# Optimization experiments

Hardware: AMD Instinct MI355X
Metric: run time of the kernel (lower is better)

## Reference

```python
import jax, jax.numpy as jnp
import numpy as np

B, N, D = 8, 2048, 512  # batch, input_dim (tokens), weight_dim


def setup_inputs() -> dict:
    key = jax.random.key(0)
    ks = jax.random.split(key, 7)
    return {
        "query": jax.random.normal(ks[0], (B, N, D), dtype=jnp.float32),
        "key": jax.random.normal(ks[1], (B, N, D), dtype=jnp.float32),
        "value": jax.random.normal(ks[2], (B, N, D), dtype=jnp.float32),
        "W_query": jax.random.normal(ks[3], (D, D), dtype=jnp.float32),
        "W_key": jax.random.normal(ks[4], (D, D), dtype=jnp.float32),
        "W_value": jax.random.normal(ks[5], (D, D), dtype=jnp.float32),
        "self_importance": jnp.zeros((N,), dtype=jnp.float32),
    }


def reference(query, key, value, W_query, W_key, W_value, self_importance):
    d = W_query.shape[0]
    q = jnp.einsum("bnd,de->bne", query, W_query)
    k = jnp.einsum("bnd,de->bne", key, W_key)
    v = jnp.einsum("bnd,de->bne", value, W_value)
    scores = jnp.einsum("bqe,bke->bqk", q, k) / jnp.sqrt(jnp.float32(d))
    # diagonal self-importance bias: eye(N) * clamp(exp(s), max=3)
    importance = jnp.minimum(jnp.exp(self_importance), 3.0)  # [N]
    n = scores.shape[1]
    idx = jnp.arange(n)
    scores = scores.at[:, idx, idx].add(importance)
    attn = jax.nn.softmax(scores, axis=-1)  # [B, N, N]
    entropy_loss = -jnp.mean(jnp.sum(attn * jnp.log(attn + 1e-10), axis=-1))
    out = jnp.einsum("bqk,bke->bqe", attn, v)
    return (out, attn, entropy_loss)
```

## Files before the change

kernel.cpp:

```cpp
#include <hip/hip_runtime.h>
#include <math.h>

#define BB 8
#define NN 2048
#define DD 512

typedef _Float16 halfT;
typedef _Float16 half8 __attribute__((ext_vector_type(8)));
typedef _Float16 half4 __attribute__((ext_vector_type(4)));
typedef float f32x4 __attribute__((ext_vector_type(4)));
typedef float f32x16 __attribute__((ext_vector_type(16)));

#define GLOAD16(gp, sp) __builtin_amdgcn_global_load_lds( \
    (const __attribute__((address_space(1))) void*)(gp), \
    (__attribute__((address_space(3))) void*)(sp), 16, 0, 0)

__global__ __launch_bounds__(256) void wsplit_kernel(
    const float* __restrict__ Wq, const float* __restrict__ Wk, const float* __restrict__ Wv,
    _Float16* __restrict__ qhT, _Float16* __restrict__ qlT,
    _Float16* __restrict__ khT, _Float16* __restrict__ klT,
    _Float16* __restrict__ vhT)
{
    __shared__ float t[64][65];
    const int z = blockIdx.z;
    const float* W = (z == 0) ? Wq : ((z == 1) ? Wk : Wv);
    _Float16* Ph = (z == 0) ? qhT : ((z == 1) ? khT : vhT);
    _Float16* Pl = (z == 0) ? qlT : ((z == 1) ? klT : nullptr);
    const int bx = blockIdx.x * 64, by = blockIdx.y * 64;
    const int tid = threadIdx.x;
    #pragma unroll
    for (int i = 0; i < 16; ++i) {
        const int idx = i * 256 + tid;
        const int r = idx >> 6, c = idx & 63;
        t[r][c] = W[(long)(by + r) * 512 + bx + c];
    }
    __syncthreads();
    #pragma unroll
    for (int i = 0; i < 16; ++i) {
        const int idx = i * 256 + tid;
        const int r = idx >> 6, c = idx & 63;
        const float v = t[c][r];
        const _Float16 h = (_Float16)v;
        const long o = (long)(bx + r) * 512 + by + c;
        Ph[o] = h;
        if (z < 2) Pl[o] = (_Float16)(v - (float)h);
    }
}

__global__ __launch_bounds__(256) void projqk_kernel(
    const float* __restrict__ Af0, const float* __restrict__ Af1,
    const _Float16* __restrict__ B0h, const _Float16* __restrict__ B0l,
    const _Float16* __restrict__ B1h, const _Float16* __restrict__ B1l,
    _Float16* __restrict__ O0h, _Float16* __restrict__ O0l,
    _Float16* __restrict__ O1h, _Float16* __restrict__ O1l)
{
    __shared__ __align__(16) _Float16 smem[4 * 128 * 32];
    _Float16* Ah = smem;
    _Float16* Bh = smem + 4096;
    _Float16* Al = smem + 8192;
    _Float16* Bl = smem + 12288;

    const int z = blockIdx.z;
    const float* Af = z ? Af1 : Af0;
    const _Float16* Bgh = z ? B1h : B0h;
    const _Float16* Bgl = z ? B1l : B0l;
    _Float16* Oh = z ? O1h : O0h;
    _Float16* Ol = z ? O1l : O0l;

    const int tid  = threadIdx.x;
    const int lane = tid & 63;
    const int w    = tid >> 6;
    const int wr   = w >> 1, wc = w & 1;
    const int bm   = blockIdx.y * 128, bn = blockIdx.x * 128;

    f32x4 acc[4][4];
    #pragma unroll
    for (int i = 0; i < 4; ++i)
        #pragma unroll
        for (int j = 0; j < 4; ++j) acc[i][j] = (f32x4)0.0f;

    for (int k0 = 0; k0 < DD; k0 += 32) {
        #pragma unroll
        for (int i = 0; i < 2; ++i) {
            const int c   = i * 256 + w * 64 + lane;
            const int row = c >> 2, sl = c & 3;
            const long g  = (long)(bn + row) * DD + k0 + sl * 8;
            const int lb  = (i * 256 + w * 64) * 8;
            GLOAD16(Bgh + g, Bh + lb);
            GLOAD16(Bgl + g, Bl + lb);
        }
        #pragma unroll
        for (int i = 0; i < 4; ++i) {
            const int c = tid + i * 256;
            const int row = c >> 3, q4 = c & 7;
            const float4 v = *(const float4*)(Af + (long)(bm + row) * DD + k0 + q4 * 4);
            half4 h;
            h[0] = (_Float16)v.x; h[1] = (_Float16)v.y;
            h[2] = (_Float16)v.z; h[3] = (_Float16)v.w;
            *(half4*)&Ah[row * 32 + q4 * 4] = h;
            half4 l;
            l[0] = (_Float16)(v.x - (float)h[0]);
            l[1] = (_Float16)(v.y - (float)h[1]);
            l[2] = (_Float16)(v.z - (float)h[2]);
            l[3] = (_Float16)(v.w - (float)h[3]);
            *(half4*)&Al[row * 32 + q4 * 4] = l;
        }
        __syncthreads();

        half8 ah[4], bh[4], al[4], bl[4];
        #pragma unroll
        for (int f = 0; f < 4; ++f) {
            const int ar = wr * 64 + f * 16 + (lane & 15);
            const int ao = ar * 32 + ((lane >> 4) << 3);
            ah[f] = *(const half8*)&Ah[ao];
            al[f] = *(const half8*)&Al[ao];
            const int br = wc * 64 + f * 16 + (lane & 15);
            const int bo = br * 32 + ((lane >> 4) << 3);
            bh[f] = *(const half8*)&Bh[bo];
            bl[f] = *(const half8*)&Bl[bo];
        }
        #pragma unroll
        for (int i = 0; i < 4; ++i)
            #pragma unroll
            for (int j = 0; j < 4; ++j) {
                acc[i][j] = __builtin_amdgcn_mfma_f32_16x16x32_f16(ah[i], bh[j], acc[i][j], 0, 0, 0);
                acc[i][j] = __builtin_amdgcn_mfma_f32_16x16x32_f16(ah[i], bl[j], acc[i][j], 0, 0, 0);
                acc[i][j] = __builtin_amdgcn_mfma_f32_16x16x32_f16(al[i], bh[j], acc[i][j], 0, 0, 0);
            }
        __syncthreads();
    }

    #pragma unroll
    for (int i = 0; i < 4; ++i) {
        const int rb = bm + wr * 64 + i * 16 + ((lane >> 4) << 2);
        #pragma unroll
        for (int j = 0; j < 4; ++j) {
            const int gc = bn + wc * 64 + j * 16 + (lane & 15);
            #pragma unroll
            for (int r = 0; r < 4; ++r) {
                const float vv = acc[i][j][r];
                const _Float16 h = (_Float16)vv;
                const long o = (long)(rb + r) * DD + gc;
                Oh[o] = h;
                Ol[o] = (_Float16)(vv - (float)h);
            }
        }
    }
}

__global__ __launch_bounds__(256) void vproj_kernel(
    const float* __restrict__ Af, const _Float16* __restrict__ Bgh,
    _Float16* __restrict__ Oh)
{
    __shared__ __align__(16) _Float16 smem[2 * 128 * 32];
    _Float16* Ah = smem;
    _Float16* Bh = smem + 4096;

    const int tid  = threadIdx.x;
    const int lane = tid & 63;
    const int w    = tid >> 6;
    const int wr   = w >> 1, wc = w & 1;
    const int bm   = blockIdx.y * 128, bn = blockIdx.x * 128;

    f32x4 acc[4][4];
    #pragma unroll
    for (int i = 0; i < 4; ++i)
        #pragma unroll
        for (int j = 0; j < 4; ++j) acc[i][j] = (f32x4)0.0f;

    for (int k0 = 0; k0 < DD; k0 += 32) {
        #pragma unroll
        for (int i = 0; i < 2; ++i) {
            const int c   = i * 256 + w * 64 + lane;
            const int row = c >> 2, sl = c & 3;
            const long g  = (long)(bn + row) * DD + k0 + sl * 8;
            const int lb  = (i * 256 + w * 64) * 8;
            GLOAD16(Bgh + g, Bh + lb);
        }
        #pragma unroll
        for (int i = 0; i < 4; ++i) {
            const int c = tid + i * 256;
            const int row = c >> 3, q4 = c & 7;
            const float4 v = *(const float4*)(Af + (long)(bm + row) * DD + k0 + q4 * 4);
            half4 h;
            h[0] = (_Float16)v.x; h[1] = (_Float16)v.y;
            h[2] = (_Float16)v.z; h[3] = (_Float16)v.w;
            *(half4*)&Ah[row * 32 + q4 * 4] = h;
        }
        __syncthreads();

        half8 ah[4], bh[4];
        #pragma unroll
        for (int f = 0; f < 4; ++f) {
            const int ar = wr * 64 + f * 16 + (lane & 15);
            ah[f] = *(const half8*)&Ah[ar * 32 + ((lane >> 4) << 3)];
            const int br = wc * 64 + f * 16 + (lane & 15);
            bh[f] = *(const half8*)&Bh[br * 32 + ((lane >> 4) << 3)];
        }
        #pragma unroll
        for (int i = 0; i < 4; ++i)
            #pragma unroll
            for (int j = 0; j < 4; ++j)
                acc[i][j] = __builtin_amdgcn_mfma_f32_16x16x32_f16(ah[i], bh[j], acc[i][j], 0, 0, 0);
        __syncthreads();
    }

    #pragma unroll
    for (int i = 0; i < 4; ++i) {
        const int rb = bm + wr * 64 + i * 16 + ((lane >> 4) << 2);
        #pragma unroll
        for (int j = 0; j < 4; ++j) {
            const int gc = bn + wc * 64 + j * 16 + (lane & 15);
            half4 hv;
            #pragma unroll
            for (int r = 0; r < 4; ++r) hv[r] = (_Float16)acc[i][j][r];
            const int b = rb >> 11, rIn = rb & 2047;
            *(half4*)&Oh[((long)b * 512 + gc) * 2048 + rIn] = hv;
        }
    }
}

__global__ __launch_bounds__(512, 2) void scores256_kernel(
    const halfT* __restrict__ qh, const halfT* __restrict__ ql,
    const halfT* __restrict__ kh, const halfT* __restrict__ kl,
    float* __restrict__ C, const float* __restrict__ si, float scale)
{
    extern __shared__ __align__(16) char smem[];

    const int tid  = threadIdx.x;
    const int lane = tid & 63;
    const int w    = tid >> 6;
    const int wr   = w >> 2, wc = w & 3;

    int flat = (blockIdx.z << 6) | (blockIdx.y << 3) | blockIdx.x;
    flat = ((flat & 7) << 6) | (flat >> 3);
    const int bx = flat & 7, by = (flat >> 3) & 7, bz = flat >> 6;
    const int bm = by * 256, bn = bx * 256;

    const long zoff = (long)bz * NN * DD;
    const halfT* A_h = qh + zoff;
    const halfT* A_l = ql + zoff;
    const halfT* B_h = kh + zoff;
    const halfT* B_l = kl + zoff;

    const int s_row   = w * 16 + (lane >> 2);
    const int s_chunk = (lane & 3) ^ ((lane >> 3) & 3);
    const long gA = (long)(bm + s_row) * DD + s_chunk * 8;
    const long gB = (long)(bn + s_row) * DD + s_chunk * 8;
    const int ldst = w * 1024;
    const long rstep = (long)128 * DD;

    auto stage = [&](char* buf, int t) {
        const long kk = (long)t * 32;
        GLOAD16(A_h + gA + kk,         buf + ldst);
        GLOAD16(A_h + gA + rstep + kk, buf + 8192 + ldst);
        GLOAD16(A_l + gA + kk,         buf + 16384 + ldst);
        GLOAD16(A_l + gA + rstep + kk, buf + 16384 + 8192 + ldst);
        GLOAD16(B_h + gB + kk,         buf + 32768 + ldst);
        GLOAD16(B_h + gB + rstep + kk, buf + 32768 + 8192 + ldst);
        GLOAD16(B_l + gB + kk,         buf + 49152 + ldst);
        GLOAD16(B_l + gB + rstep + kk, buf + 49152 + 8192 + ldst);
    };

    const int frow = lane & 31;
    const int fgr  = lane >> 5;

    f32x16 acc[4][2];
    #pragma unroll
    for (int m = 0; m < 4; ++m)
        #pragma unroll
        for (int n = 0; n < 2; ++n) acc[m][n] = (f32x16)0.0f;

    stage(smem, 0);
    asm volatile("s_waitcnt vmcnt(0)" ::: "memory");
    __builtin_amdgcn_s_barrier();
    __builtin_amdgcn_sched_barrier(0);

    for (int t = 0; t < 16; ++t) {
        char* cur = smem + (size_t)(t & 1) * 65536;
        char* nxt = smem + (size_t)((t + 1) & 1) * 65536;

        if (t < 15) stage(nxt, t + 1);

        auto fr = [&](const char* unit, int row, int kh) -> half8 {
            const int g = kh * 2 + fgr;
            const int phys = g ^ ((row >> 1) & 3);
            return *(const half8*)(unit + row * 64 + phys * 16);
        };

        half8 a_[4][2], bh_[2][2];
        #pragma unroll
        for (int kh2 = 0; kh2 < 2; ++kh2) {
            #pragma unroll
            for (int n = 0; n < 2; ++n)
                bh_[n][kh2] = fr(cur + 32768, wc * 64 + n * 32 + frow, kh2);
            #pragma unroll
            for (int m = 0; m < 4; ++m)
                a_[m][kh2] = fr(cur, wr * 128 + m * 32 + frow, kh2);
        }
        __builtin_amdgcn_s_setprio(1);
        #pragma unroll
        for (int m = 0; m < 4; ++m)
            #pragma unroll
            for (int n = 0; n < 2; ++n)
                #pragma unroll
                for (int kh2 = 0; kh2 < 2; ++kh2)
                    acc[m][n] = __builtin_amdgcn_mfma_f32_32x32x16_f16(a_[m][kh2], bh_[n][kh2], acc[m][n], 0, 0, 0);
        __builtin_amdgcn_s_setprio(0);

        half8 bl_[2][2];
        #pragma unroll
        for (int kh2 = 0; kh2 < 2; ++kh2)
            #pragma unroll
            for (int n = 0; n < 2; ++n)
                bl_[n][kh2] = fr(cur + 49152, wc * 64 + n * 32 + frow, kh2);
        __builtin_amdgcn_s_setprio(1);
        #pragma unroll
        for (int m = 0; m < 4; ++m)
            #pragma unroll
            for (int n = 0; n < 2; ++n)
                #pragma unroll
                for (int kh2 = 0; kh2 < 2; ++kh2)
                    acc[m][n] = __builtin_amdgcn_mfma_f32_32x32x16_f16(a_[m][kh2], bl_[n][kh2], acc[m][n], 0, 0, 0);
        __builtin_amdgcn_s_setprio(0);

        __builtin_amdgcn_s_setprio(1);
        #pragma unroll
        for (int m = 0; m < 4; ++m) {
            half8 al0 = fr(cur + 16384, wr * 128 + m * 32 + frow, 0);
            half8 al1 = fr(cur + 16384, wr * 128 + m * 32 + frow, 1);
            #pragma unroll
            for (int n = 0; n < 2; ++n) {
                acc[m][n] = __builtin_amdgcn_mfma_f32_32x32x16_f16(al0, bh_[n][0], acc[m][n], 0, 0, 0);
                acc[m][n] = __builtin_amdgcn_mfma_f32_32x32x16_f16(al1, bh_[n][1], acc[m][n], 0, 0, 0);
            }
        }
        __builtin_amdgcn_s_setprio(0);

        if (t < 15) {
            asm volatile("s_waitcnt vmcnt(0)" ::: "memory");
            __builtin_amdgcn_s_barrier();
        }
    }

    float* Cz = C + (long)bz * NN * NN;
    const int rbias = 4 * (lane >> 5);
    #pragma unroll
    for (int m = 0; m < 4; ++m) {
        #pragma unroll
        for (int n = 0; n < 2; ++n) {
            const int gc = bn + wc * 64 + n * 32 + (lane & 31);
            #pragma unroll
            for (int reg = 0; reg < 16; ++reg) {
                const int gr = bm + wr * 128 + m * 32 + (reg & 3) + 8 * (reg >> 2) + rbias;
                float vv = acc[m][n][reg] * scale;
                if (gr == gc) vv += fminf(expf(si[gr]), 3.0f);
                Cz[(long)gr * NN + gc] = vv;
            }
        }
    }
}

__global__ __launch_bounds__(512, 2) void av_kernel(
    const halfT* __restrict__ P, const halfT* __restrict__ V,
    float* __restrict__ O)
{
    extern __shared__ __align__(16) char smem[];

    const int tid  = threadIdx.x;
    const int lane = tid & 63;
    const int w    = tid >> 6;
    const int wr   = w >> 2, wc = w & 3;

    int flat = (blockIdx.z << 5) | (blockIdx.y << 2) | blockIdx.x;
    flat = ((flat & 7) << 5) | (flat >> 3);
    const int nx = flat & 3, my = (flat >> 2) & 7, bz = flat >> 5;
    const int bm = my * 256, bn = nx * 128;

    const halfT* A = P + (long)bz * NN * NN;
    const halfT* B = V + (long)bz * DD * NN;

    const int s_row   = w * 16 + (lane >> 2);
    const int s_chunk = (lane & 3) ^ ((lane >> 3) & 3);
    const long gA = (long)(bm + s_row) * NN + s_chunk * 8;
    const long gB = (long)(bn + s_row) * NN + s_chunk * 8;
    const int ldst = w * 1024;
    const long rstep = (long)128 * NN;

    auto stage = [&](char* buf, int t) {
        const long kk = (long)t * 32;
        GLOAD16(A + gA + kk,         buf + ldst);
        GLOAD16(A + gA + rstep + kk, buf + 8192 + ldst);
        GLOAD16(B + gB + kk,         buf + 16384 + ldst);
    };

    const int frow = lane & 31;
    const int fgr  = lane >> 5;

    f32x16 acc[4];
    #pragma unroll
    for (int m = 0; m < 4; ++m) acc[m] = (f32x16)0.0f;

    stage(smem, 0);
    asm volatile("s_waitcnt vmcnt(0)" ::: "memory");
    __builtin_amdgcn_s_barrier();
    __builtin_amdgcn_sched_barrier(0);

    for (int t = 0; t < 64; ++t) {
        char* cur = smem + (size_t)(t & 1) * 24576;
        char* nxt = smem + (size_t)((t + 1) & 1) * 24576;

        if (t < 63) stage(nxt, t + 1);

        auto fr = [&](const char* unit, int row, int kh) -> half8 {
            const int g = kh * 2 + fgr;
            const int phys = g ^ ((row >> 1) & 3);
            return *(const half8*)(unit + row * 64 + phys * 16);
        };

        half8 a_[4][2], b_[2];
        #pragma unroll
        for (int kh2 = 0; kh2 < 2; ++kh2) {
            b_[kh2] = fr(cur + 16384, wc * 32 + frow, kh2);
            #pragma unroll
            for (int m = 0; m < 4; ++m)
                a_[m][kh2] = fr(cur, wr * 128 + m * 32 + frow, kh2);
        }
        __builtin_amdgcn_s_setprio(1);
        #pragma unroll
        for (int m = 0; m < 4; ++m)
            #pragma unroll
            for (int kh2 = 0; kh2 < 2; ++kh2)
                acc[m] = __builtin_amdgcn_mfma_f32_32x32x16_f16(a_[m][kh2], b_[kh2], acc[m], 0, 0, 0);
        __builtin_amdgcn_s_setprio(0);

        if (t < 63) {
            asm volatile("s_waitcnt vmcnt(0)" ::: "memory");
            __builtin_amdgcn_s_barrier();
        }
    }

    float* Oz = O + (long)bz * NN * DD;
    const int rbias = 4 * (lane >> 5);
    const int gc = bn + wc * 32 + (lane & 31);
    #pragma unroll
    for (int m = 0; m < 4; ++m) {
        #pragma unroll
        for (int reg = 0; reg < 16; ++reg) {
            const int gr = bm + wr * 128 + m * 32 + (reg & 3) + 8 * (reg >> 2) + rbias;
            Oz[(long)gr * DD + gc] = acc[m][reg];
        }
    }
}

__global__ __launch_bounds__(256) void softmax_entropy_kernel(
    float* __restrict__ attn, _Float16* __restrict__ ah, float* __restrict__ partials)
{
    __shared__ float red[4];
    const long row = blockIdx.x;
    float* p = attn + row * (long)NN;
    _Float16* ph = ah + row * (long)NN;
    const int tid = threadIdx.x;
    const int base = tid * 8;

    float4 va = *(const float4*)(p + base);
    float4 vb = *(const float4*)(p + base + 4);
    float v[8] = {va.x, va.y, va.z, va.w, vb.x, vb.y, vb.z, vb.w};

    float m = v[0];
    #pragma unroll
    for (int i = 1; i < 8; ++i) m = fmaxf(m, v[i]);
    #pragma unroll
    for (int o = 32; o; o >>= 1) m = fmaxf(m, __shfl_xor(m, o, 64));
    if ((tid & 63) == 0) red[tid >> 6] = m;
    __syncthreads();
    m = fmaxf(fmaxf(red[0], red[1]), fmaxf(red[2], red[3]));

    float t[8];
    float s = 0.f;
    #pragma unroll
    for (int i = 0; i < 8; ++i) { t[i] = v[i] - m; v[i] = expf(t[i]); s += v[i]; }
    #pragma unroll
    for (int o = 32; o; o >>= 1) s += __shfl_xor(s, o, 64);
    __syncthreads();
    if ((tid & 63) == 0) red[tid >> 6] = s;
    __syncthreads();
    s = red[0] + red[1] + red[2] + red[3];

    const float inv = 1.0f / s;
    const float lns = logf(s);
    float e = 0.f;
    float pv[8];
    #pragma unroll
    for (int i = 0; i < 8; ++i) {
        pv[i] = v[i] * inv;
        e = fmaf(pv[i], t[i] - lns, e);
    }
    *(float4*)(p + base)     = make_float4(pv[0], pv[1], pv[2], pv[3]);
    *(float4*)(p + base + 4) = make_float4(pv[4], pv[5], pv[6], pv[7]);
    half8 h;
    #pragma unroll
    for (int i = 0; i < 8; ++i) h[i] = (_Float16)pv[i];
    *(half8*)(ph + base) = h;

    #pragma unroll
    for (int o = 32; o; o >>= 1) e += __shfl_xor(e, o, 64);
    __syncthreads();
    if ((tid & 63) == 0) red[tid >> 6] = e;
    __syncthreads();
    if (tid == 0) partials[row] = red[0] + red[1] + red[2] + red[3];
}

__global__ __launch_bounds__(256) void ent_reduce_kernel(
    const float* __restrict__ partials, float* __restrict__ ent)
{
    __shared__ float red[4];
    float s = 0.f;
    for (int i = threadIdx.x; i < BB * NN; i += 256) s += partials[i];
    #pragma unroll
    for (int o = 32; o; o >>= 1) s += __shfl_xor(s, o, 64);
    if ((threadIdx.x & 63) == 0) red[threadIdx.x >> 6] = s;
    __syncthreads();
    if (threadIdx.x == 0)
        *ent = -(red[0] + red[1] + red[2] + red[3]) / (float)(BB * NN);
}

extern "C" void kernel_launch(void* const* d_in, const int* in_sizes, int n_in,
                              void* d_out, int out_size, void* d_ws, size_t ws_size,
                              hipStream_t stream) {
    const float* query = (const float*)d_in[0];
    const float* key   = (const float*)d_in[1];
    const float* value = (const float*)d_in[2];
    const float* Wq    = (const float*)d_in[3];
    const float* Wk    = (const float*)d_in[4];
    const float* Wv    = (const float*)d_in[5];
    const float* si    = (const float*)d_in[6];

    float* out  = (float*)d_out;
    float* attn = out + (size_t)BB * NN * DD;
    float* ent  = attn + (size_t)BB * NN * NN;

    const size_t NK = (size_t)BB * NN * DD;
    _Float16* ws16 = (_Float16*)d_ws;
    _Float16* qh = ws16;
    _Float16* ql = qh + NK;
    _Float16* kh = ql + NK;
    _Float16* kl = kh + NK;
    _Float16* vT = kl + NK;
    _Float16* WqhT = vT + NK;
    _Float16* WqlT = WqhT + DD * DD;
    _Float16* WkhT = WqlT + DD * DD;
    _Float16* WklT = WkhT + DD * DD;
    _Float16* WvhT = WklT + DD * DD;
    float* partials = (float*)(WvhT + DD * DD);
    _Float16* attn_h = ws16;

    const dim3 blk(256);
    const float inv_sqrt_d = 0.044194173824159216f;

    wsplit_kernel<<<dim3(8, 8, 3), blk, 0, stream>>>(Wq, Wk, Wv,
        WqhT, WqlT, WkhT, WklT, WvhT);

    projqk_kernel<<<dim3(4, 128, 2), blk, 0, stream>>>(
        query, key, WqhT, WqlT, WkhT, WklT, qh, ql, kh, kl);
    vproj_kernel<<<dim3(4, 128, 1), blk, 0, stream>>>(value, WvhT, vT);

    scores256_kernel<<<dim3(8, 8, 8), dim3(512), 131072, stream>>>(
        qh, ql, kh, kl, attn, si, inv_sqrt_d);

    softmax_entropy_kernel<<<dim3(BB * NN), blk, 0, stream>>>(attn, attn_h, partials);
    ent_reduce_kernel<<<dim3(1), blk, 0, stream>>>(partials, ent);

    av_kernel<<<dim3(4, 8, 8), dim3(512), 49152, stream>>>(attn_h, vT, out);
}
```

Before: 335.0 us.

## Rework Q/K projection pipeline and switch scores/AV MFMAs to 16x16 tiles

```diff
diff --git a/kernel.cpp b/kernel.cpp
--- a/kernel.cpp
+++ b/kernel.cpp
@@ -9,7 +9,6 @@
 typedef _Float16 half8 __attribute__((ext_vector_type(8)));
 typedef _Float16 half4 __attribute__((ext_vector_type(4)));
 typedef float f32x4 __attribute__((ext_vector_type(4)));
-typedef float f32x16 __attribute__((ext_vector_type(16)));
 
 #define GLOAD16(gp, sp) __builtin_amdgcn_global_load_lds( \
     (const __attribute__((address_space(1))) void*)(gp), \
@@ -47,25 +46,169 @@
     }
 }
 
-__global__ __launch_bounds__(256) void projqk_kernel(
-    const float* __restrict__ Af0, const float* __restrict__ Af1,
-    const _Float16* __restrict__ B0h, const _Float16* __restrict__ B0l,
-    const _Float16* __restrict__ B1h, const _Float16* __restrict__ B1l,
-    _Float16* __restrict__ O0h, _Float16* __restrict__ O0l,
-    _Float16* __restrict__ O1h, _Float16* __restrict__ O1l)
+__global__ __launch_bounds__(512, 2) void projqk_kernel(
+    const float* __restrict__ X0, const float* __restrict__ X1,
+    const halfT* __restrict__ B0h, const halfT* __restrict__ B0l,
+    const halfT* __restrict__ B1h, const halfT* __restrict__ B1l,
+    halfT* __restrict__ O0h, halfT* __restrict__ O0l,
+    halfT* __restrict__ O1h, halfT* __restrict__ O1l)
 {
-    __shared__ __align__(16) _Float16 smem[4 * 128 * 32];
+    extern __shared__ __align__(16) char smem[];
+
+    const int tid  = threadIdx.x;
+    const int lane = tid & 63;
+    const int w    = tid >> 6;
+    const int wr   = w >> 1, wc = w & 1;
+
+    const int h = blockIdx.x;
+    const int L = ((h & 7) << 6) | (h >> 3);
+    const int z  = L >> 8;
+    const int nx = L & 3, my = (L >> 2) & 63;
+    const int bm = my * 256, bn = nx * 128;
+
+    const float* X = z ? X1 : X0;
+    const halfT* Bgh = z ? B1h : B0h;
+    const halfT* Bgl = z ? B1l : B0l;
+    halfT* Oh = z ? O1h : O0h;
+    halfT* Ol = z ? O1l : O0l;
+
+    const int b_row   = w * 16 + (lane >> 2);
+    const int b_chunk = (lane & 3) ^ ((lane >> 3) & 3);
+    const long gB = (long)(bn + b_row) * DD + b_chunk * 8;
+    const int ldstB = w * 1024;
+
+    const int a_row0 = tid >> 2;
+    const int a_gc   = tid & 3;
+    const int a_phys = a_gc ^ ((a_row0 >> 1) & 3);
+    const long gA0 = (long)(bm + a_row0) * DD + a_gc * 8;
+    const long gA1 = (long)(bm + a_row0 + 128) * DD + a_gc * 8;
+    const int aOff0 = a_row0 * 64 + a_phys * 16;
+    const int aOff1 = (a_row0 + 128) * 64 + a_phys * 16;
+
+    float ar[16];
+    auto loadA = [&](int t) {
+        const long kk = (long)t * 32;
+        *(float4*)&ar[0]  = *(const float4*)(X + gA0 + kk);
+        *(float4*)&ar[4]  = *(const float4*)(X + gA0 + kk + 4);
+        *(float4*)&ar[8]  = *(const float4*)(X + gA1 + kk);
+        *(float4*)&ar[12] = *(const float4*)(X + gA1 + kk + 4);
+    };
+    auto stageB = [&](char* buf, int t) {
+        const long kk = (long)t * 32;
+        GLOAD16(Bgh + gB + kk, buf + 32768 + ldstB);
+        GLOAD16(Bgl + gB + kk, buf + 40960 + ldstB);
+    };
+    auto writeA = [&](char* buf) {
+        half8 h0, l0, h1, l1;
+        #pragma unroll
+        for (int i = 0; i < 8; ++i) {
+            const _Float16 hh = (_Float16)ar[i];
+            h0[i] = hh; l0[i] = (_Float16)(ar[i] - (float)hh);
+        }
+        #pragma unroll
+        for (int i = 0; i < 8; ++i) {
+            const _Float16 hh = (_Float16)ar[8 + i];
+            h1[i] = hh; l1[i] = (_Float16)(ar[8 + i] - (float)hh);
+        }
+        *(half8*)(buf + aOff0)         = h0;
+        *(half8*)(buf + 16384 + aOff0) = l0;
+        *(half8*)(buf + aOff1)         = h1;
+        *(half8*)(buf + 16384 + aOff1) = l1;
+    };
+
+    const int lr  = lane & 15;
+    const int q16 = lane >> 4;
+    const int frag = lr * 64 + ((q16 ^ ((lr >> 1) & 3)) << 4);
+    const int abase = wr * 4096 + frag;
+    const int bbase = wc * 4096 + frag;
+
+    f32x4 acc[4][4];
+    #pragma unroll
+    for (int i = 0; i < 4; ++i)
+        #pragma unroll
+        for (int j = 0; j < 4; ++j) acc[i][j] = (f32x4)0.0f;
+
+    loadA(0);
+    stageB(smem, 0);
+    writeA(smem);
+    asm volatile("s_waitcnt vmcnt(0) lgkmcnt(0)" ::: "memory");
+    __builtin_amdgcn_s_barrier();
+    __builtin_amdgcn_sched_barrier(0);
+
+    for (int t = 0; t < 16; ++t) {
+        char* cur = smem + (size_t)(t & 1) * 49152;
+        char* nxt = smem + (size_t)((t + 1) & 1) * 49152;
+        const bool pf = (t < 15);
+
+        if (pf) { loadA(t + 1); stageB(nxt, t + 1); }
+
+        half8 ah[4], bh[4], bl[4];
+        #pragma unroll
+        for (int m = 0; m < 4; ++m)
+            ah[m] = *(const half8*)(cur + abase + m * 1024);
+        #pragma unroll
+        for (int j = 0; j < 4; ++j)
+            bh[j] = *(const half8*)(cur + 32768 + bbase + j * 1024);
+        __builtin_amdgcn_s_setprio(1);
+        #pragma unroll
+        for (int m = 0; m < 4; ++m)
+            #pragma unroll
+            for (int j = 0; j < 4; ++j)
+                acc[m][j] = __builtin_amdgcn_mfma_f32_16x16x32_f16(ah[m], bh[j], acc[m][j], 0, 0, 0);
+        __builtin_amdgcn_s_setprio(0);
+
+        #pragma unroll
+        for (int j = 0; j < 4; ++j)
+            bl[j] = *(const half8*)(cur + 40960 + bbase + j * 1024);
+        __builtin_amdgcn_s_setprio(1);
+        #pragma unroll
+        for (int m = 0; m < 4; ++m)
+            #pragma unroll
+            for (int j = 0; j < 4; ++j)
+                acc[m][j] = __builtin_amdgcn_mfma_f32_16x16x32_f16(ah[m], bl[j], acc[m][j], 0, 0, 0);
+        __builtin_amdgcn_s_setprio(0);
+
+        __builtin_amdgcn_s_setprio(1);
+        #pragma unroll
+        for (int m = 0; m < 4; ++m) {
+            const half8 al = *(const half8*)(cur + 16384 + abase + m * 1024);
+            #pragma unroll
+            for (int j = 0; j < 4; ++j)
+                acc[m][j] = __builtin_amdgcn_mfma_f32_16x16x32_f16(al, bh[j], acc[m][j], 0, 0, 0);
+        }
+        __builtin_amdgcn_s_setprio(0);
+
+        if (pf) writeA(nxt);
+        asm volatile("s_waitcnt vmcnt(0) lgkmcnt(0)" ::: "memory");
+        __builtin_amdgcn_s_barrier();
+        __builtin_amdgcn_sched_barrier(0);
+    }
+
+    #pragma unroll
+    for (int m = 0; m < 4; ++m) {
+        const int rb = bm + wr * 64 + m * 16 + (q16 << 2);
+        #pragma unroll
+        for (int j = 0; j < 4; ++j) {
+            const int gc = bn + wc * 64 + j * 16 + lr;
+            #pragma unroll
+            for (int r = 0; r < 4; ++r) {
+                const float vv = acc[m][j][r];
+                const _Float16 hh = (_Float16)vv;
+                const long o = (long)(rb + r) * DD + gc;
+                Oh[o] = hh;
+                Ol[o] = (_Float16)(vv - (float)hh);
+            }
+        }
+    }
+}
+
+__global__ __launch_bounds__(256) void vproj_kernel(
+    const float* __restrict__ Af, const _Float16* __restrict__ Bgh,
+    _Float16* __restrict__ Oh)
+{
+    __shared__ __align__(16) _Float16 smem[2 * 128 * 32];
     _Float16* Ah = smem;
     _Float16* Bh = smem + 4096;
-    _Float16* Al = smem + 8192;
-    _Float16* Bl = smem + 12288;
-
-    const int z = blockIdx.z;
-    const float* Af = z ? Af1 : Af0;
-    const _Float16* Bgh = z ? B1h : B0h;
-    const _Float16* Bgl = z ? B1l : B0l;
-    _Float16* Oh = z ? O1h : O0h;
-    _Float16* Ol = z ? O1l : O0l;
 
     const int tid  = threadIdx.x;
     const int lane = tid & 63;
@@ -87,7 +230,6 @@
             const long g  = (long)(bn + row) * DD + k0 + sl * 8;
             const int lb  = (i * 256 + w * 64) * 8;
             GLOAD16(Bgh + g, Bh + lb);
-            GLOAD16(Bgl + g, Bl + lb);
         }
         #pragma unroll
         for (int i = 0; i < 4; ++i) {
@@ -98,104 +240,16 @@
             h[0] = (_Float16)v.x; h[1] = (_Float16)v.y;
             h[2] = (_Float16)v.z; h[3] = (_Float16)v.w;
             *(half4*)&Ah[row * 32 + q4 * 4] = h;
-            half4 l;
-            l[0] = (_Float16)(v.x - (float)h[0]);
-            l[1] = (_Float16)(v.y - (float)h[1]);
-            l[2] = (_Float16)(v.z - (float)h[2]);
-            l[3] = (_Float16)(v.w - (float)h[3]);
-            *(half4*)&Al[row * 32 + q4 * 4] = l;
         }
         __syncthreads();
 
-        half8 ah[4], bh[4], al[4], bl[4];
+        half8 ah[4], bh[4];
         #pragma unroll
         for (int f = 0; f < 4; ++f) {
-            const int ar = wr * 64 + f * 16 + (lane & 15);
-            const int ao = ar * 32 + ((lane >> 4) << 3);
-            ah[f] = *(const half8*)&Ah[ao];
-            al[f] = *(const half8*)&Al[ao];
-            const int br = wc * 64 + f * 16 + (lane & 15);
-            const int bo = br * 32 + ((lane >> 4) << 3);
-            bh[f] = *(const half8*)&Bh[bo];
-            bl[f] = *(const half8*)&Bl[bo];
-        }
-        #pragma unroll
-        for (int i = 0; i < 4; ++i)
-            #pragma unroll
-            for (int j = 0; j < 4; ++j) {
-                acc[i][j] = __builtin_amdgcn_mfma_f32_16x16x32_f16(ah[i], bh[j], acc[i][j], 0, 0, 0);
-                acc[i][j] = __builtin_amdgcn_mfma_f32_16x16x32_f16(ah[i], bl[j], acc[i][j], 0, 0, 0);
-                acc[i][j] = __builtin_amdgcn_mfma_f32_16x16x32_f16(al[i], bh[j], acc[i][j], 0, 0, 0);
-            }
-        __syncthreads();
-    }
-
-    #pragma unroll
-    for (int i = 0; i < 4; ++i) {
-        const int rb = bm + wr * 64 + i * 16 + ((lane >> 4) << 2);
-        #pragma unroll
-        for (int j = 0; j < 4; ++j) {
-            const int gc = bn + wc * 64 + j * 16 + (lane & 15);
-            #pragma unroll
-            for (int r = 0; r < 4; ++r) {
-                const float vv = acc[i][j][r];
-                const _Float16 h = (_Float16)vv;
-                const long o = (long)(rb + r) * DD + gc;
-                Oh[o] = h;
-                Ol[o] = (_Float16)(vv - (float)h);
-            }
-        }
-    }
-}
-
-__global__ __launch_bounds__(256) void vproj_kernel(
-    const float* __restrict__ Af, const _Float16* __restrict__ Bgh,
-    _Float16* __restrict__ Oh)
-{
-    __shared__ __align__(16) _Float16 smem[2 * 128 * 32];
-    _Float16* Ah = smem;
-    _Float16* Bh = smem + 4096;
-
-    const int tid  = threadIdx.x;
-    const int lane = tid & 63;
-    const int w    = tid >> 6;
-    const int wr   = w >> 1, wc = w & 1;
-    const int bm   = blockIdx.y * 128, bn = blockIdx.x * 128;
-
-    f32x4 acc[4][4];
-    #pragma unroll
-    for (int i = 0; i < 4; ++i)
-        #pragma unroll
-        for (int j = 0; j < 4; ++j) acc[i][j] = (f32x4)0.0f;
-
-    for (int k0 = 0; k0 < DD; k0 += 32) {
-        #pragma unroll
-        for (int i = 0; i < 2; ++i) {
-            const int c   = i * 256 + w * 64 + lane;
-            const int row = c >> 2, sl = c & 3;
-            const long g  = (long)(bn + row) * DD + k0 + sl * 8;
-            const int lb  = (i * 256 + w * 64) * 8;
-            GLOAD16(Bgh + g, Bh + lb);
-        }
-        #pragma unroll
-        for (int i = 0; i < 4; ++i) {
-            const int c = tid + i * 256;
-            const int row = c >> 3, q4 = c & 7;
-            const float4 v = *(const float4*)(Af + (long)(bm + row) * DD + k0 + q4 * 4);
-            half4 h;
-            h[0] = (_Float16)v.x; h[1] = (_Float16)v.y;
-            h[2] = (_Float16)v.z; h[3] = (_Float16)v.w;
-            *(half4*)&Ah[row * 32 + q4 * 4] = h;
-        }
-        __syncthreads();
-
-        half8 ah[4], bh[4];
-        #pragma unroll
-        for (int f = 0; f < 4; ++f) {
-            const int ar = wr * 64 + f * 16 + (lane & 15);
-            ah[f] = *(const half8*)&Ah[ar * 32 + ((lane >> 4) << 3)];
-            const int br = wc * 64 + f * 16 + (lane & 15);
-            bh[f] = *(const half8*)&Bh[br * 32 + ((lane >> 4) << 3)];
+            const int arr = wr * 64 + f * 16 + (lane & 15);
+            ah[f] = *(const half8*)&Ah[arr * 32 + ((lane >> 4) << 3)];
+            const int brr = wc * 64 + f * 16 + (lane & 15);
+            bh[f] = *(const half8*)&Bh[brr * 32 + ((lane >> 4) << 3)];
         }
         #pragma unroll
         for (int i = 0; i < 4; ++i)
@@ -262,19 +316,22 @@
         GLOAD16(B_l + gB + rstep + kk, buf + 49152 + 8192 + ldst);
     };
 
-    const int frow = lane & 31;
-    const int fgr  = lane >> 5;
-
-    f32x16 acc[4][2];
-    #pragma unroll
-    for (int m = 0; m < 4; ++m)
-        #pragma unroll
-        for (int n = 0; n < 2; ++n) acc[m][n] = (f32x16)0.0f;
+    const int lr   = lane & 15;
+    const int q16  = lane >> 4;
+    const int fswz = (lr >> 1) & 3;
+    const int frag = lr * 64 + ((q16 ^ fswz) << 4);
+    const int abase = wr * 8192 + frag;
+    const int bbase = wc * 4096 + frag;
+
+    f32x4 acc[8][4];
+    #pragma unroll
+    for (int m = 0; m < 8; ++m)
+        #pragma unroll
+        for (int n = 0; n < 4; ++n) acc[m][n] = (f32x4)0.0f;
 
     stage(smem, 0);
     asm volatile("s_waitcnt vmcnt(0)" ::: "memory");
     __builtin_amdgcn_s_barrier();
-    __builtin_amdgcn_sched_barrier(0);
 
     for (int t = 0; t < 16; ++t) {
         char* cur = smem + (size_t)(t & 1) * 65536;
@@ -282,58 +339,39 @@
 
         if (t < 15) stage(nxt, t + 1);
 
-        auto fr = [&](const char* unit, int row, int kh) -> half8 {
-            const int g = kh * 2 + fgr;
-            const int phys = g ^ ((row >> 1) & 3);
-            return *(const half8*)(unit + row * 64 + phys * 16);
-        };
-
-        half8 a_[4][2], bh_[2][2];
-        #pragma unroll
-        for (int kh2 = 0; kh2 < 2; ++kh2) {
-            #pragma unroll
-            for (int n = 0; n < 2; ++n)
-                bh_[n][kh2] = fr(cur + 32768, wc * 64 + n * 32 + frow, kh2);
-            #pragma unroll
-            for (int m = 0; m < 4; ++m)
-                a_[m][kh2] = fr(cur, wr * 128 + m * 32 + frow, kh2);
-        }
+        half8 ah[8], bh[4], bl[4];
+        #pragma unroll
+        for (int n = 0; n < 4; ++n)
+            bh[n] = *(const half8*)(cur + 32768 + bbase + n * 1024);
+        #pragma unroll
+        for (int m = 0; m < 8; ++m)
+            ah[m] = *(const half8*)(cur + abase + m * 1024);
         __builtin_amdgcn_s_setprio(1);
         #pragma unroll
-        for (int m = 0; m < 4; ++m)
-            #pragma unroll
-            for (int n = 0; n < 2; ++n)
-                #pragma unroll
-                for (int kh2 = 0; kh2 < 2; ++kh2)
-                    acc[m][n] = __builtin_amdgcn_mfma_f32_32x32x16_f16(a_[m][kh2], bh_[n][kh2], acc[m][n], 0, 0, 0);
+        for (int m = 0; m < 8; ++m)
+            #pragma unroll
+            for (int n = 0; n < 4; ++n)
+                acc[m][n] = __builtin_amdgcn_mfma_f32_16x16x32_f16(ah[m], bh[n], acc[m][n], 0, 0, 0);
         __builtin_amdgcn_s_setprio(0);
 
-        half8 bl_[2][2];
-        #pragma unroll
-        for (int kh2 = 0; kh2 < 2; ++kh2)
-            #pragma unroll
-            for (int n = 0; n < 2; ++n)
-                bl_[n][kh2] = fr(cur + 49152, wc * 64 + n * 32 + frow, kh2);
+        #pragma unroll
+        for (int n = 0; n < 4; ++n)
+            bl[n] = *(const half8*)(cur + 49152 + bbase + n * 1024);
         __builtin_amdgcn_s_setprio(1);
         #pragma unroll
-        for (int m = 0; m < 4; ++m)
-            #pragma unroll
-            for (int n = 0; n < 2; ++n)
-                #pragma unroll
-                for (int kh2 = 0; kh2 < 2; ++kh2)
-                    acc[m][n] = __builtin_amdgcn_mfma_f32_32x32x16_f16(a_[m][kh2], bl_[n][kh2], acc[m][n], 0, 0, 0);
+        for (int m = 0; m < 8; ++m)
+            #pragma unroll
+            for (int n = 0; n < 4; ++n)
+                acc[m][n] = __builtin_amdgcn_mfma_f32_16x16x32_f16(ah[m], bl[n], acc[m][n], 0, 0, 0);
         __builtin_amdgcn_s_setprio(0);
 
         __builtin_amdgcn_s_setprio(1);
         #pragma unroll
-        for (int m = 0; m < 4; ++m) {
-            half8 al0 = fr(cur + 16384, wr * 128 + m * 32 + frow, 0);
-            half8 al1 = fr(cur + 16384, wr * 128 + m * 32 + frow, 1);
-            #pragma unroll
-            for (int n = 0; n < 2; ++n) {
-                acc[m][n] = __builtin_amdgcn_mfma_f32_32x32x16_f16(al0, bh_[n][0], acc[m][n], 0, 0, 0);
-                acc[m][n] = __builtin_amdgcn_mfma_f32_32x32x16_f16(al1, bh_[n][1], acc[m][n], 0, 0, 0);
-            }
+        for (int m = 0; m < 8; ++m) {
+            const half8 al = *(const half8*)(cur + 16384 + abase + m * 1024);
+            #pragma unroll
+            for (int n = 0; n < 4; ++n)
+                acc[m][n] = __builtin_amdgcn_mfma_f32_16x16x32_f16(al, bh[n], acc[m][n], 0, 0, 0);
         }
         __builtin_amdgcn_s_setprio(0);
 
@@ -344,16 +382,16 @@
     }
 
     float* Cz = C + (long)bz * NN * NN;
-    const int rbias = 4 * (lane >> 5);
-    #pragma unroll
-    for (int m = 0; m < 4; ++m) {
-        #pragma unroll
-        for (int n = 0; n < 2; ++n) {
-            const int gc = bn + wc * 64 + n * 32 + (lane & 31);
-            #pragma unroll
-            for (int reg = 0; reg < 16; ++reg) {
-                const int gr = bm + wr * 128 + m * 32 + (reg & 3) + 8 * (reg >> 2) + rbias;
-                float vv = acc[m][n][reg] * scale;
+    #pragma unroll
+    for (int m = 0; m < 8; ++m) {
+        const int rb = bm + wr * 128 + m * 16 + ((lane >> 4) << 2);
+        #pragma unroll
+        for (int n = 0; n < 4; ++n) {
+            const int gc = bn + wc * 64 + n * 16 + (lane & 15);
+            #pragma unroll
+            for (int r = 0; r < 4; ++r) {
+                const int gr = rb + r;
+                float vv = acc[m][n][r] * scale;
                 if (gr == gc) vv += fminf(expf(si[gr]), 3.0f);
                 Cz[(long)gr * NN + gc] = vv;
             }
@@ -370,9 +408,9 @@
     const int tid  = threadIdx.x;
     const int lane = tid & 63;
     const int w    = tid >> 6;
-    const int wr   = w >> 2, wc = w & 3;
-
-    int flat = (blockIdx.z << 5) | (blockIdx.y << 2) | blockIdx.x;
+    const int wr   = w >> 1, wc = w & 1;
+
+    int flat = blockIdx.x;
     flat = ((flat & 7) << 5) | (flat >> 3);
     const int nx = flat & 3, my = (flat >> 2) & 7, bz = flat >> 5;
     const int bm = my * 256, bn = nx * 128;
@@ -394,12 +432,17 @@
         GLOAD16(B + gB + kk,         buf + 16384 + ldst);
     };
 
-    const int frow = lane & 31;
-    const int fgr  = lane >> 5;
-
-    f32x16 acc[4];
-    #pragma unroll
-    for (int m = 0; m < 4; ++m) acc[m] = (f32x16)0.0f;
+    const int lr  = lane & 15;
+    const int q16 = lane >> 4;
+    const int frag = lr * 64 + ((q16 ^ ((lr >> 1) & 3)) << 4);
+    const int abase = wr * 4096 + frag;
+    const int bbase = wc * 4096 + frag;
+
+    f32x4 acc[4][4];
+    #pragma unroll
+    for (int m = 0; m < 4; ++m)
+        #pragma unroll
+        for (int j = 0; j < 4; ++j) acc[m][j] = (f32x4)0.0f;
 
     stage(smem, 0);
     asm volatile("s_waitcnt vmcnt(0)" ::: "memory");
@@ -412,26 +455,19 @@
 
         if (t < 63) stage(nxt, t + 1);
 
-        auto fr = [&](const char* unit, int row, int kh) -> half8 {
-            const int g = kh * 2 + fgr;
-            const int phys = g ^ ((row >> 1) & 3);
-            return *(const half8*)(unit + row * 64 + phys * 16);
-        };
-
-        half8 a_[4][2], b_[2];
-        #pragma unroll
-        for (int kh2 = 0; kh2 < 2; ++kh2) {
-            b_[kh2] = fr(cur + 16384, wc * 32 + frow, kh2);
-            #pragma unroll
-            for (int m = 0; m < 4; ++m)
-                a_[m][kh2] = fr(cur, wr * 128 + m * 32 + frow, kh2);
-        }
+        half8 ah[4], bh[4];
+        #pragma unroll
+        for (int m = 0; m < 4; ++m)
+            ah[m] = *(const half8*)(cur + abase + m * 1024);
+        #pragma unroll
+        for (int j = 0; j < 4; ++j)
+            bh[j] = *(const half8*)(cur + 16384 + bbase + j * 1024);
         __builtin_amdgcn_s_setprio(1);
         #pragma unroll
         for (int m = 0; m < 4; ++m)
             #pragma unroll
-            for (int kh2 = 0; kh2 < 2; ++kh2)
-                acc[m] = __builtin_amdgcn_mfma_f32_32x32x16_f16(a_[m][kh2], b_[kh2], acc[m], 0, 0, 0);
+            for (int j = 0; j < 4; ++j)
+                acc[m][j] = __builtin_amdgcn_mfma_f32_16x16x32_f16(ah[m], bh[j], acc[m][j], 0, 0, 0);
         __builtin_amdgcn_s_setprio(0);
 
         if (t < 63) {
@@ -441,14 +477,15 @@
     }
 
     float* Oz = O + (long)bz * NN * DD;
-    const int rbias = 4 * (lane >> 5);
-    const int gc = bn + wc * 32 + (lane & 31);
     #pragma unroll
     for (int m = 0; m < 4; ++m) {
-        #pragma unroll
-        for (int reg = 0; reg < 16; ++reg) {
-            const int gr = bm + wr * 128 + m * 32 + (reg & 3) + 8 * (reg >> 2) + rbias;
-            Oz[(long)gr * DD + gc] = acc[m][reg];
+        const int rb = bm + wr * 64 + m * 16 + (q16 << 2);
+        #pragma unroll
+        for (int j = 0; j < 4; ++j) {
+            const int gc = bn + wc * 64 + j * 16 + lr;
+            #pragma unroll
+            for (int r = 0; r < 4; ++r)
+                Oz[(long)(rb + r) * DD + gc] = acc[m][j][r];
         }
     }
 }
@@ -561,7 +598,7 @@
     wsplit_kernel<<<dim3(8, 8, 3), blk, 0, stream>>>(Wq, Wk, Wv,
         WqhT, WqlT, WkhT, WklT, WvhT);
 
-    projqk_kernel<<<dim3(4, 128, 2), blk, 0, stream>>>(
+    projqk_kernel<<<dim3(512), dim3(512), 98304, stream>>>(
         query, key, WqhT, WqlT, WkhT, WklT, qh, ql, kh, kl);
     vproj_kernel<<<dim3(4, 128, 1), blk, 0, stream>>>(value, WvhT, vT);
 
@@ -571,5 +608,5 @@
     softmax_entropy_kernel<<<dim3(BB * NN), blk, 0, stream>>>(attn, attn_h, partials);
     ent_reduce_kernel<<<dim3(1), blk, 0, stream>>>(partials, ent);
 
-    av_kernel<<<dim3(4, 8, 8), dim3(512), 49152, stream>>>(attn_h, vT, out);
-}
+    av_kernel<<<dim3(256), dim3(512), 49152, stream>>>(attn_h, vT, out);
+}
```

Result: faster. 314.4 us (-6.1%).
